# Performance work log

Measured on AMD Instinct MI355X. Metric: run time of the kernel, lower is better.

The kernel has to match this reference:

```python
import jax, jax.numpy as jnp
import numpy as np
from jax.ops import segment_sum, segment_max

N, E, IN_DIM, HID, HEADS, B, ACTIONS = 16384, 262144, 512, 256, 4, 64, 32
NEG_SLOPE = 0.2  # PyG GATConv default leaky-relu slope


def setup_inputs() -> dict:
    key = jax.random.key(0)
    ks = jax.random.split(key, 12)
    x = jax.random.normal(ks[0], (N, IN_DIM), dtype=jnp.float32)
    edge_index = jax.random.randint(ks[1], (2, E), 0, N, dtype=jnp.int64)
    batch = jnp.sort(jax.random.randint(ks[2], (N,), 0, B, dtype=jnp.int64))
    s = 0.05
    return {
        "x": x,
        "edge_index": edge_index,
        "batch": batch,
        # SAGEConv: lin_l (neighbors, with bias) + lin_r (root, no bias)
        "sage_w_l": jax.random.normal(ks[3], (IN_DIM, HID), dtype=jnp.float32) * s,
        "sage_b_l": jnp.zeros((HID,), dtype=jnp.float32),
        "sage_w_r": jax.random.normal(ks[4], (IN_DIM, HID), dtype=jnp.float32) * s,
        # GATConv: shared lin, per-head attention vectors, output bias (concat=False)
        "gat_w": jax.random.normal(ks[5], (HID, HEADS * HID), dtype=jnp.float32) * s,
        "gat_att_src": jax.random.normal(ks[6], (HEADS, HID), dtype=jnp.float32) * s,
        "gat_att_dst": jax.random.normal(ks[7], (HEADS, HID), dtype=jnp.float32) * s,
        "gat_b": jnp.zeros((HID,), dtype=jnp.float32),
        # action head
        "head_w": jax.random.normal(ks[8], (HID, ACTIONS), dtype=jnp.float32) * s,
        "head_b": jnp.zeros((ACTIONS,), dtype=jnp.float32),
    }


def reference(x, edge_index, batch, sage_w_l, sage_b_l, sage_w_r,
              gat_w, gat_att_src, gat_att_dst, gat_b, head_w, head_b):
    src, dst = edge_index[0], edge_index[1]

    # ---- SAGEConv (mean aggregation): lin_l(mean_j x_j) + lin_r(x_i) ----
    agg = segment_sum(x[src], dst, num_segments=N)                 # [N, IN_DIM]
    deg = segment_sum(jnp.ones((E,), x.dtype), dst, num_segments=N)
    mean_nbr = agg / jnp.maximum(deg, 1.0)[:, None]
    h = mean_nbr @ sage_w_l + sage_b_l + x @ sage_w_r              # [N, HID]
    h = jax.nn.relu(h)
    # dropout is identity at inference (training=False)

    # ---- GATConv (adds self-loops, concat=False -> head average) ----
    loop = jnp.arange(N, dtype=src.dtype)
    si = jnp.concatenate([src, loop])                              # [E2]
    di = jnp.concatenate([dst, loop])
    g = (h @ gat_w).reshape(N, HEADS, HID)                         # [N, H, C]
    a_src = jnp.einsum('nhc,hc->nh', g, gat_att_src)               # [N, H]
    a_dst = jnp.einsum('nhc,hc->nh', g, gat_att_dst)
    logits = jax.nn.leaky_relu(a_src[si] + a_dst[di], NEG_SLOPE)   # [E2, H]
    m = segment_max(logits, di, num_segments=N)                    # per-target max
    ex = jnp.exp(logits - m[di])
    denom = segment_sum(ex, di, num_segments=N)
    alpha = ex / denom[di]                                         # [E2, H]
    out = segment_sum(g[si] * alpha[:, :, None], di, num_segments=N)  # [N, H, C]
    out = jax.nn.relu(out.mean(axis=1) + gat_b)                    # [N, HID]

    # ---- global mean pool + action head ----
    pooled = segment_sum(out, batch, num_segments=B)
    cnt = segment_sum(jnp.ones((N,), out.dtype), batch, num_segments=B)
    pooled = pooled / jnp.maximum(cnt, 1.0)[:, None]               # [B, HID]
    return pooled @ head_w + head_b                                # [B, ACTIONS]
```

## Files before the change

kernel.cpp:

```cpp
#include <hip/hip_runtime.h>
#include <math.h>

#define N_NODES 16384
#define N_EDGES 262144
#define IN_DIM  512
#define HID     256
#define HEADS   4
#define NBATCH  64
#define ACTIONS 32
#define NEG_SLOPE 0.2f

typedef __attribute__((ext_vector_type(8))) short short8;
typedef __attribute__((ext_vector_type(4))) float f32x4;

__device__ __forceinline__ float lrelu(float v) { return v > 0.f ? v : NEG_SLOPE * v; }

__device__ __forceinline__ unsigned short bf16_rne(float f) {
    union { float f; unsigned int u; } x; x.f = f;
    unsigned int u = x.u;
    unsigned int r = (u + 0x7FFFu + ((u >> 16) & 1u)) >> 16;
    return (unsigned short)r;
}

__device__ __forceinline__ float bf16_to_f32(unsigned short s) {
    union { unsigned int u; float f; } x; x.u = (unsigned int)s << 16;
    return x.f;
}

__device__ __forceinline__ float4 bf4_to_f4(ushort4 u) {
    return make_float4(bf16_to_f32(u.x), bf16_to_f32(u.y), bf16_to_f32(u.z), bf16_to_f32(u.w));
}

__device__ __forceinline__ void async_copy16(const unsigned short* g, unsigned short* l) {
    __builtin_amdgcn_global_load_lds(
        (const __attribute__((address_space(1))) unsigned int*)g,
        (__attribute__((address_space(3))) unsigned int*)l, 16, 0, 0);
}

#define NB_CONV 8192
#define NB_WLR  1024
#define NB_WSTK 1024
#define NB_WATT 8
#define NB_ZERO 128
#define NB_SETUP (NB_CONV + NB_WLR + NB_WSTK + NB_WATT + NB_ZERO)

__global__ __launch_bounds__(256) void setup_kernel(
        const float* __restrict__ x, unsigned short* __restrict__ xb,
        const float* __restrict__ wl, const float* __restrict__ wr, unsigned short* __restrict__ bt1,
        const float* __restrict__ gat_w, unsigned short* __restrict__ bt2,
        const float* __restrict__ att_src, const float* __restrict__ att_dst, float* __restrict__ watt,
        int* __restrict__ deg, float* __restrict__ pooled) {
    int bid = blockIdx.x, tid = threadIdx.x;
    if (bid < NB_CONV) {
        int i = (bid * 256 + tid) * 4;
        float4 v = *(const float4*)(x + i);
        ushort4 o;
        o.x = bf16_rne(v.x); o.y = bf16_rne(v.y); o.z = bf16_rne(v.z); o.w = bf16_rne(v.w);
        *(ushort4*)(xb + i) = o;
    } else if (bid < NB_CONV + NB_WLR) {
        int idx = (bid - NB_CONV) * 256 + tid;
        int j = idx >> 9;
        int k = idx & 511;
        float v = (j < HID) ? wl[k * HID + j] : wr[k * HID + (j - HID)];
        bt1[idx] = bf16_rne(v);
    } else if (bid < NB_CONV + NB_WLR + NB_WSTK) {
        int idx = (bid - NB_CONV - NB_WLR) * 256 + tid;
        int c = idx >> 10;
        int r = idx & 1023;
        int h = r >> 8;
        int k = r & 255;
        bt2[idx] = bf16_rne(gat_w[(size_t)k * (HEADS * HID) + h * HID + c]);
    } else if (bid < NB_CONV + NB_WLR + NB_WSTK + NB_WATT) {
        int j = bid - NB_CONV - NB_WLR - NB_WSTK;
        int c = tid;
        int hh = j & 3;
        const float* att = (j < 4) ? (att_src + hh * HID) : (att_dst + hh * HID);
        float s = 0.f;
        for (int cc = 0; cc < HID; cc++)
            s += gat_w[(size_t)c * (HEADS * HID) + hh * HID + cc] * att[cc];
        watt[j * HID + c] = s;
    } else {
        int idx = (bid - NB_CONV - NB_WLR - NB_WSTK - NB_WATT) * 256 + tid;
        if (idx < N_NODES) deg[idx] = 0;
        else pooled[idx - N_NODES] = 0.f;
    }
}

__global__ void deg_kernel(const int* __restrict__ ei, int* __restrict__ deg) {
    int e = blockIdx.x * 256 + threadIdx.x;
    if (e < N_EDGES) atomicAdd(&deg[ei[N_EDGES + e]], 1);
}

__global__ __launch_bounds__(256) void scan_kernel(const int* __restrict__ deg,
                                                   int* __restrict__ row_start,
                                                   int* __restrict__ pos) {
    int t = threadIdx.x;
    int lane = t & 63, wv = t >> 6;
    int base = t * 64;
    int4 buf[16];
    int sum = 0;
#pragma unroll
    for (int i = 0; i < 16; i++) {
        buf[i] = ((const int4*)(deg + base))[i];
        sum += buf[i].x + buf[i].y + buf[i].z + buf[i].w;
    }
    int v = sum;
#pragma unroll
    for (int off = 1; off < 64; off <<= 1) {
        int u = __shfl_up(v, off);
        if (lane >= off) v += u;
    }
    __shared__ int wsum[4];
    if (lane == 63) wsum[wv] = v;
    __syncthreads();
    int wbase = 0;
    for (int w0 = 0; w0 < wv; w0++) wbase += wsum[w0];
    int run = wbase + v - sum;
#pragma unroll
    for (int i = 0; i < 16; i++) {
        int4 b = buf[i];
        int4 o;
        o.x = run; run += b.x;
        o.y = run; run += b.y;
        o.z = run; run += b.z;
        o.w = run; run += b.w;
        ((int4*)(row_start + base))[i] = o;
        ((int4*)(pos + base))[i] = o;
    }
    if (t == 255) row_start[N_NODES] = run;
}

__global__ void fill_kernel(const int* __restrict__ ei, int* __restrict__ pos,
                            int* __restrict__ col) {
    int e = blockIdx.x * 256 + threadIdx.x;
    if (e < N_EDGES) {
        int s = ei[e];
        int d = ei[N_EDGES + e];
        int p = atomicAdd(&pos[d], 1);
        col[p] = s;
    }
}

#define BK 32

__global__ __launch_bounds__(256) void gemm1_kernel(const unsigned short* __restrict__ A,
                                                    const unsigned short* __restrict__ Bt,
                                                    unsigned short* __restrict__ Cb,
                                                    int Nn, int K) {
    __shared__ __align__(16) unsigned short As[64 * BK];
    __shared__ __align__(16) unsigned short Bs[128 * BK];

    int tid  = threadIdx.x;
    int wv   = tid >> 6;
    int lane = tid & 63;
    int m0 = blockIdx.y * 64;
    int n0 = blockIdx.x * 128;
    int wm = (wv & 1) * 32;
    int wn = (wv >> 1) * 64;

    int srow = tid >> 2;
    int scol = (tid & 3) * 8;
    const unsigned short* Ag  = A  + (size_t)(m0 + srow) * K + scol;
    const unsigned short* Bg0 = Bt + (size_t)(n0 + srow) * K + scol;
    const unsigned short* Bg1 = Bt + (size_t)(n0 + 64 + srow) * K + scol;
    unsigned short* Al  = As + wv * 512;
    unsigned short* Bl0 = Bs + wv * 512;
    unsigned short* Bl1 = Bs + 2048 + wv * 512;

    int fr = lane & 15;
    int fk = (lane >> 4) * 8;
    f32x4 acc[2][4] = {};

    for (int kt = 0; kt < K; kt += BK) {
        async_copy16(Ag + kt, Al);
        async_copy16(Bg0 + kt, Bl0);
        async_copy16(Bg1 + kt, Bl1);
        __syncthreads();

        short8 af[2], bf[4];
#pragma unroll
        for (int mi = 0; mi < 2; mi++)
            af[mi] = *(const short8*)&As[(wm + mi * 16 + fr) * BK + fk];
#pragma unroll
        for (int ni = 0; ni < 4; ni++)
            bf[ni] = *(const short8*)&Bs[(wn + ni * 16 + fr) * BK + fk];
#pragma unroll
        for (int mi = 0; mi < 2; mi++)
#pragma unroll
            for (int ni = 0; ni < 4; ni++)
                acc[mi][ni] = __builtin_amdgcn_mfma_f32_16x16x32_bf16(af[mi], bf[ni], acc[mi][ni], 0, 0, 0);
        __syncthreads();
    }

    int cr = (lane >> 4) * 4;
    int cc = lane & 15;
#pragma unroll
    for (int mi = 0; mi < 2; mi++) {
#pragma unroll
        for (int ni = 0; ni < 4; ni++) {
            int gc = n0 + wn + ni * 16 + cc;
#pragma unroll
            for (int r = 0; r < 4; r++) {
                int gr = m0 + wm + mi * 16 + cr + r;
                Cb[(size_t)gr * Nn + gc] = bf16_rne(acc[mi][ni][r]);
            }
        }
    }
}

__global__ __launch_bounds__(256) void gemm2_pool_kernel(const unsigned short* __restrict__ A,
                                                         const unsigned short* __restrict__ Bt,
                                                         const int* __restrict__ batch,
                                                         const float* __restrict__ bias,
                                                         float scale,
                                                         float* __restrict__ pooled,
                                                         int Nn, int K) {
    __shared__ __align__(16) unsigned short As[64 * BK];
    __shared__ __align__(16) unsigned short Bs[64 * BK];
    __shared__ int bsh[64];

    int tid  = threadIdx.x;
    int wv   = tid >> 6;
    int lane = tid & 63;
    int m0 = blockIdx.y * 64;
    int n0 = blockIdx.x * 64;
    int wm = (wv & 1) * 32;
    int wn = (wv >> 1) * 32;

    if (tid < 64) bsh[tid] = batch[m0 + tid];

    int srow = tid >> 2;
    int scol = (tid & 3) * 8;
    const unsigned short* Ag = A  + (size_t)(m0 + srow) * K + scol;
    const unsigned short* Bg = Bt + (size_t)(n0 + srow) * K + scol;
    unsigned short* Al = As + wv * 512;
    unsigned short* Bl = Bs + wv * 512;

    int fr = lane & 15;
    int fk = (lane >> 4) * 8;
    f32x4 acc[2][2] = {};

    for (int kt = 0; kt < K; kt += BK) {
        async_copy16(Ag + kt, Al);
        async_copy16(Bg + kt, Bl);
        __syncthreads();

        short8 af[2], bf[2];
#pragma unroll
        for (int mi = 0; mi < 2; mi++)
            af[mi] = *(const short8*)&As[(wm + mi * 16 + fr) * BK + fk];
#pragma unroll
        for (int ni = 0; ni < 2; ni++)
            bf[ni] = *(const short8*)&Bs[(wn + ni * 16 + fr) * BK + fk];
#pragma unroll
        for (int mi = 0; mi < 2; mi++)
#pragma unroll
            for (int ni = 0; ni < 2; ni++)
                acc[mi][ni] = __builtin_amdgcn_mfma_f32_16x16x32_bf16(af[mi], bf[ni], acc[mi][ni], 0, 0, 0);
        __syncthreads();
    }

    int cr = (lane >> 4) * 4;
    int cc = lane & 15;
#pragma unroll
    for (int mi = 0; mi < 2; mi++) {
        int rowb = wm + mi * 16 + cr;
        int b0 = bsh[rowb], b3 = bsh[rowb + 3];
#pragma unroll
        for (int ni = 0; ni < 2; ni++) {
            int gc = n0 + wn + ni * 16 + cc;
            float b = bias[gc];
            float v0 = fmaxf(fmaf(acc[mi][ni][0], scale, b), 0.f);
            float v1 = fmaxf(fmaf(acc[mi][ni][1], scale, b), 0.f);
            float v2 = fmaxf(fmaf(acc[mi][ni][2], scale, b), 0.f);
            float v3 = fmaxf(fmaf(acc[mi][ni][3], scale, b), 0.f);
            if (b0 == b3) {
                atomicAdd(&pooled[b0 * HID + gc], (v0 + v1) + (v2 + v3));
            } else {
                atomicAdd(&pooled[bsh[rowb + 0] * HID + gc], v0);
                atomicAdd(&pooled[bsh[rowb + 1] * HID + gc], v1);
                atomicAdd(&pooled[bsh[rowb + 2] * HID + gc], v2);
                atomicAdd(&pooled[bsh[rowb + 3] * HID + gc], v3);
            }
        }
    }
}

__global__ __launch_bounds__(256) void sage_agg_kernel(const unsigned short* __restrict__ xlr,
                                                       const int* __restrict__ row_start,
                                                       const int* __restrict__ col,
                                                       const float* __restrict__ b_l,
                                                       const float* __restrict__ watt,
                                                       unsigned short* __restrict__ hb,
                                                       float* __restrict__ a_att) {
    __shared__ float watt_s[8 * HID];
    for (int i = threadIdx.x; i < 8 * HID; i += 256) watt_s[i] = watt[i];
    __syncthreads();

    int wave = threadIdx.x >> 6;
    int lane = threadIdx.x & 63;
    int n = blockIdx.x * 4 + wave;
    int start = row_start[n], end = row_start[n + 1];
    int c0 = lane * 4;

    float4 acc = make_float4(0.f, 0.f, 0.f, 0.f);
    int e = start;
    for (; e + 4 <= end; e += 4) {
        int s0 = col[e], s1 = col[e + 1], s2 = col[e + 2], s3 = col[e + 3];
        ushort4 u0 = *(const ushort4*)(xlr + (size_t)s0 * IN_DIM + c0);
        ushort4 u1 = *(const ushort4*)(xlr + (size_t)s1 * IN_DIM + c0);
        ushort4 u2 = *(const ushort4*)(xlr + (size_t)s2 * IN_DIM + c0);
        ushort4 u3 = *(const ushort4*)(xlr + (size_t)s3 * IN_DIM + c0);
        float4 v0 = bf4_to_f4(u0), v1 = bf4_to_f4(u1), v2 = bf4_to_f4(u2), v3 = bf4_to_f4(u3);
        acc.x += (v0.x + v1.x) + (v2.x + v3.x);
        acc.y += (v0.y + v1.y) + (v2.y + v3.y);
        acc.z += (v0.z + v1.z) + (v2.z + v3.z);
        acc.w += (v0.w + v1.w) + (v2.w + v3.w);
    }
    for (; e < end; e++) {
        int s = col[e];
        float4 v = bf4_to_f4(*(const ushort4*)(xlr + (size_t)s * IN_DIM + c0));
        acc.x += v.x; acc.y += v.y; acc.z += v.z; acc.w += v.w;
    }
    float inv = 1.f / (float)max(end - start, 1);
    float4 xr = bf4_to_f4(*(const ushort4*)(xlr + (size_t)n * IN_DIM + HID + c0));
    float4 bl = *(const float4*)(b_l + c0);
    float4 hv;
    hv.x = fmaxf(fmaf(acc.x, inv, bl.x + xr.x), 0.f);
    hv.y = fmaxf(fmaf(acc.y, inv, bl.y + xr.y), 0.f);
    hv.z = fmaxf(fmaf(acc.z, inv, bl.z + xr.z), 0.f);
    hv.w = fmaxf(fmaf(acc.w, inv, bl.w + xr.w), 0.f);
    ushort4 ho;
    ho.x = bf16_rne(hv.x); ho.y = bf16_rne(hv.y); ho.z = bf16_rne(hv.z); ho.w = bf16_rne(hv.w);
    *(ushort4*)(hb + (size_t)n * HID + c0) = ho;

    float p[8];
#pragma unroll
    for (int j = 0; j < 8; j++) {
        float4 wt = *(const float4*)&watt_s[j * HID + c0];
        p[j] = hv.x * wt.x + hv.y * wt.y + hv.z * wt.z + hv.w * wt.w;
    }
#pragma unroll
    for (int off = 32; off; off >>= 1)
#pragma unroll
        for (int j = 0; j < 8; j++) p[j] += __shfl_down(p[j], off);
    if (lane == 0) {
#pragma unroll
        for (int j = 0; j < 8; j++) a_att[n * 8 + j] = p[j];
    }
}

__global__ __launch_bounds__(256) void gat_agg_kernel(const unsigned short* __restrict__ hb,
                                                      const float* __restrict__ a_att,
                                                      const int* __restrict__ row_start,
                                                      const int* __restrict__ col,
                                                      unsigned short* __restrict__ T) {
    __shared__ __align__(16) float w_s[4][64 * 4];
    int wave = threadIdx.x >> 6;
    int lane = threadIdx.x & 63;
    int n = blockIdx.x * 4 + wave;
    int start = row_start[n], end = row_start[n + 1];

    float4 an = *(const float4*)(a_att + n * 8);
    float4 ad = *(const float4*)(a_att + n * 8 + 4);
    float adst[4] = {ad.x, ad.y, ad.z, ad.w};
    float selfl[4] = {lrelu(an.x + ad.x), lrelu(an.y + ad.y), lrelu(an.z + ad.z), lrelu(an.w + ad.w)};
    float m[4], wself[4];
#pragma unroll
    for (int hh = 0; hh < 4; hh++) {
        m[hh] = fmaxf(selfl[hh], 0.f);
        wself[hh] = __expf(selfl[hh] - m[hh]);
    }

    int c0 = lane * 4;
    float4 hn = bf4_to_f4(*(const ushort4*)(hb + (size_t)n * HID + c0));
    float4 acc[4];
#pragma unroll
    for (int hh = 0; hh < 4; hh++)
        acc[hh] = make_float4(wself[hh] * hn.x, wself[hh] * hn.y, wself[hh] * hn.z, wself[hh] * hn.w);

    float dpart[4] = {0.f, 0.f, 0.f, 0.f};

    for (int base = start; base < end; base += 64) {
        int cnt = min(64, end - base);
        if (lane < cnt) {
            int s = col[base + lane];
            float4 as = *(const float4*)(a_att + s * 8);
            float4 wv;
            wv.x = __expf(lrelu(as.x + adst[0]) - m[0]);
            wv.y = __expf(lrelu(as.y + adst[1]) - m[1]);
            wv.z = __expf(lrelu(as.z + adst[2]) - m[2]);
            wv.w = __expf(lrelu(as.w + adst[3]) - m[3]);
            *(float4*)&w_s[wave][lane * 4] = wv;
            dpart[0] += wv.x; dpart[1] += wv.y; dpart[2] += wv.z; dpart[3] += wv.w;
        }
        __builtin_amdgcn_wave_barrier();

        int i = 0;
        for (; i + 2 <= cnt; i += 2) {
            int s0 = col[base + i], s1 = col[base + i + 1];
            float4 w0 = *(const float4*)&w_s[wave][i * 4];
            float4 w1 = *(const float4*)&w_s[wave][(i + 1) * 4];
            ushort4 u0 = *(const ushort4*)(hb + (size_t)s0 * HID + c0);
            ushort4 u1 = *(const ushort4*)(hb + (size_t)s1 * HID + c0);
            float4 h0 = bf4_to_f4(u0), h1 = bf4_to_f4(u1);
            float wr0[4] = {w0.x, w0.y, w0.z, w0.w};
            float wr1[4] = {w1.x, w1.y, w1.z, w1.w};
#pragma unroll
            for (int hh = 0; hh < 4; hh++) {
                acc[hh].x = fmaf(wr0[hh], h0.x, fmaf(wr1[hh], h1.x, acc[hh].x));
                acc[hh].y = fmaf(wr0[hh], h0.y, fmaf(wr1[hh], h1.y, acc[hh].y));
                acc[hh].z = fmaf(wr0[hh], h0.z, fmaf(wr1[hh], h1.z, acc[hh].z));
                acc[hh].w = fmaf(wr0[hh], h0.w, fmaf(wr1[hh], h1.w, acc[hh].w));
            }
        }
        if (i < cnt) {
            int s0 = col[base + i];
            float4 w0 = *(const float4*)&w_s[wave][i * 4];
            float4 h0 = bf4_to_f4(*(const ushort4*)(hb + (size_t)s0 * HID + c0));
            float wr0[4] = {w0.x, w0.y, w0.z, w0.w};
#pragma unroll
            for (int hh = 0; hh < 4; hh++) {
                acc[hh].x = fmaf(wr0[hh], h0.x, acc[hh].x);
                acc[hh].y = fmaf(wr0[hh], h0.y, acc[hh].y);
                acc[hh].z = fmaf(wr0[hh], h0.z, acc[hh].z);
                acc[hh].w = fmaf(wr0[hh], h0.w, acc[hh].w);
            }
        }
        __builtin_amdgcn_wave_barrier();
    }

#pragma unroll
    for (int off = 32; off; off >>= 1)
#pragma unroll
        for (int hh = 0; hh < 4; hh++) dpart[hh] += __shfl_down(dpart[hh], off);
    float invd[4];
#pragma unroll
    for (int hh = 0; hh < 4; hh++)
        invd[hh] = 1.f / (__shfl(dpart[hh], 0) + wself[hh]);

#pragma unroll
    for (int hh = 0; hh < 4; hh++) {
        ushort4 o;
        o.x = bf16_rne(acc[hh].x * invd[hh]); o.y = bf16_rne(acc[hh].y * invd[hh]);
        o.z = bf16_rne(acc[hh].z * invd[hh]); o.w = bf16_rne(acc[hh].w * invd[hh]);
        *(ushort4*)(T + (size_t)n * (HEADS * HID) + hh * HID + c0) = o;
    }
}

__device__ __forceinline__ int lower_bound_i(const int* a, int n, int v) {
    int lo = 0, hi = n;
    while (lo < hi) {
        int mid = (lo + hi) >> 1;
        if (a[mid] < v) lo = mid + 1; else hi = mid;
    }
    return lo;
}

__global__ __launch_bounds__(256) void head_kernel(const float* __restrict__ pooled,
                                                   const int* __restrict__ batch,
                                                   const float* __restrict__ head_w,
                                                   const float* __restrict__ head_b,
                                                   float* __restrict__ out) {
    __shared__ float sm[HID];
    int b = blockIdx.x;
    int c = threadIdx.x;
    int lo = lower_bound_i(batch, N_NODES, b);
    int hi = lower_bound_i(batch, N_NODES, b + 1);
    int cnt = hi - lo;
    sm[c] = pooled[b * HID + c] / (float)max(cnt, 1);
    __syncthreads();
    if (c < ACTIONS) {
        float acc = head_b[c];
        for (int k = 0; k < HID; k++) acc = fmaf(sm[k], head_w[k * ACTIONS + c], acc);
        out[b * ACTIONS + c] = acc;
    }
}

extern "C" void kernel_launch(void* const* d_in, const int* in_sizes, int n_in,
                              void* d_out, int out_size, void* d_ws, size_t ws_size,
                              hipStream_t stream) {
    const float* x        = (const float*)d_in[0];
    const int*   ei       = (const int*)d_in[1];
    const int*   batch    = (const int*)d_in[2];
    const float* sage_w_l = (const float*)d_in[3];
    const float* sage_b_l = (const float*)d_in[4];
    const float* sage_w_r = (const float*)d_in[5];
    const float* gat_w    = (const float*)d_in[6];
    const float* att_src  = (const float*)d_in[7];
    const float* att_dst  = (const float*)d_in[8];
    const float* gat_b    = (const float*)d_in[9];
    const float* head_w   = (const float*)d_in[10];
    const float* head_b   = (const float*)d_in[11];
    float* out = (float*)d_out;

    char* w = (char*)d_ws;
    float* a_att  = (float*)w; w += (size_t)N_NODES * 8 * 4;
    float* watt   = (float*)w; w += (size_t)8 * HID * 4;
    float* pooled = (float*)w; w += (size_t)NBATCH * HID * 4;
    unsigned short* xb  = (unsigned short*)w; w += (size_t)N_NODES * IN_DIM * 2;
    unsigned short* xlr = (unsigned short*)w; w += (size_t)N_NODES * IN_DIM * 2;
    unsigned short* hb  = (unsigned short*)w; w += (size_t)N_NODES * HID * 2;
    unsigned short* T   = (unsigned short*)w; w += (size_t)N_NODES * HEADS * HID * 2;
    unsigned short* bt1 = (unsigned short*)w; w += (size_t)(2 * HID) * IN_DIM * 2;
    unsigned short* bt2 = (unsigned short*)w; w += (size_t)HID * (HEADS * HID) * 2;
    int* deg      = (int*)w;   w += (size_t)N_NODES * 4;
    int* row_start= (int*)w;   w += (size_t)(N_NODES + 64) * 4;
    int* pos      = (int*)w;   w += (size_t)N_NODES * 4;
    int* col      = (int*)w;   w += (size_t)N_EDGES * 4;

    setup_kernel<<<NB_SETUP, 256, 0, stream>>>(x, xb, sage_w_l, sage_w_r, bt1,
                                               gat_w, bt2, att_src, att_dst, watt,
                                               deg, pooled);

    deg_kernel<<<N_EDGES / 256, 256, 0, stream>>>(ei, deg);
    scan_kernel<<<1, 256, 0, stream>>>(deg, row_start, pos);
    fill_kernel<<<N_EDGES / 256, 256, 0, stream>>>(ei, pos, col);

    gemm1_kernel<<<dim3((2 * HID) / 128, N_NODES / 64), 256, 0, stream>>>(
        xb, bt1, xlr, 2 * HID, IN_DIM);

    sage_agg_kernel<<<N_NODES / 4, 256, 0, stream>>>(xlr, row_start, col, sage_b_l, watt, hb, a_att);

    gat_agg_kernel<<<N_NODES / 4, 256, 0, stream>>>(hb, a_att, row_start, col, T);

    gemm2_pool_kernel<<<dim3(HID / 64, N_NODES / 64), 256, 0, stream>>>(
        T, bt2, batch, gat_b, 0.25f, pooled, HID, HEADS * HID);

    head_kernel<<<NBATCH, 256, 0, stream>>>(pooled, batch, head_w, head_b, out);
}
```

Before: 262.4 us.

## Split GEMM2 along K with 128x128 tiles and separate relu-pool pass

Replaces the fused 64x64-tile GEMM2+pool kernel with a split-K GEMM using 128x128 tiles over four K chunks. Partial sums are atomically added into a new fp32 [N,HID] buffer, which is zeroed in the setup kernel. A separate kernel then applies bias, scale and relu and does segmented pooling. The aim is more reuse per tile while keeping enough blocks in flight, at the cost of an extra 16 MB fp32 buffer, heavy global atomics, an extra zeroing pass and an extra launch.

```diff
diff --git a/kernel.cpp b/kernel.cpp
--- a/kernel.cpp
+++ b/kernel.cpp
@@ -42,14 +42,15 @@
 #define NB_WSTK 1024
 #define NB_WATT 8
 #define NB_ZERO 128
-#define NB_SETUP (NB_CONV + NB_WLR + NB_WSTK + NB_WATT + NB_ZERO)
+#define NB_ZOUT 4096
+#define NB_SETUP (NB_CONV + NB_WLR + NB_WSTK + NB_WATT + NB_ZERO + NB_ZOUT)
 
 __global__ __launch_bounds__(256) void setup_kernel(
         const float* __restrict__ x, unsigned short* __restrict__ xb,
         const float* __restrict__ wl, const float* __restrict__ wr, unsigned short* __restrict__ bt1,
         const float* __restrict__ gat_w, unsigned short* __restrict__ bt2,
         const float* __restrict__ att_src, const float* __restrict__ att_dst, float* __restrict__ watt,
-        int* __restrict__ deg, float* __restrict__ pooled) {
+        int* __restrict__ deg, float* __restrict__ pooled, float* __restrict__ outn) {
     int bid = blockIdx.x, tid = threadIdx.x;
     if (bid < NB_CONV) {
         int i = (bid * 256 + tid) * 4;
@@ -79,10 +80,13 @@
         for (int cc = 0; cc < HID; cc++)
             s += gat_w[(size_t)c * (HEADS * HID) + hh * HID + cc] * att[cc];
         watt[j * HID + c] = s;
-    } else {
+    } else if (bid < NB_CONV + NB_WLR + NB_WSTK + NB_WATT + NB_ZERO) {
         int idx = (bid - NB_CONV - NB_WLR - NB_WSTK - NB_WATT) * 256 + tid;
         if (idx < N_NODES) deg[idx] = 0;
         else pooled[idx - N_NODES] = 0.f;
+    } else {
+        int i = ((bid - NB_CONV - NB_WLR - NB_WSTK - NB_WATT - NB_ZERO) * 256 + tid) * 4;
+        *(float4*)(outn + i) = make_float4(0.f, 0.f, 0.f, 0.f);
     }
 }
 
@@ -208,54 +212,57 @@
     }
 }
 
-__global__ __launch_bounds__(256) void gemm2_pool_kernel(const unsigned short* __restrict__ A,
-                                                         const unsigned short* __restrict__ Bt,
-                                                         const int* __restrict__ batch,
-                                                         const float* __restrict__ bias,
-                                                         float scale,
-                                                         float* __restrict__ pooled,
-                                                         int Nn, int K) {
-    __shared__ __align__(16) unsigned short As[64 * BK];
-    __shared__ __align__(16) unsigned short Bs[64 * BK];
-    __shared__ int bsh[64];
+#define KCHUNK 256
+
+__global__ __launch_bounds__(256) void gemm2_splitk_kernel(const unsigned short* __restrict__ A,
+                                                           const unsigned short* __restrict__ Bt,
+                                                           float* __restrict__ outn,
+                                                           int Nn, int K) {
+    __shared__ __align__(16) unsigned short As[128 * BK];
+    __shared__ __align__(16) unsigned short Bs[128 * BK];
 
     int tid  = threadIdx.x;
     int wv   = tid >> 6;
     int lane = tid & 63;
-    int m0 = blockIdx.y * 64;
-    int n0 = blockIdx.x * 64;
-    int wm = (wv & 1) * 32;
-    int wn = (wv >> 1) * 32;
-
-    if (tid < 64) bsh[tid] = batch[m0 + tid];
+    int m0 = blockIdx.y * 128;
+    int n0 = blockIdx.x * 128;
+    int k0 = blockIdx.z * KCHUNK;
+    int wm = (wv & 1) * 64;
+    int wn = (wv >> 1) * 64;
 
     int srow = tid >> 2;
     int scol = (tid & 3) * 8;
-    const unsigned short* Ag = A  + (size_t)(m0 + srow) * K + scol;
-    const unsigned short* Bg = Bt + (size_t)(n0 + srow) * K + scol;
-    unsigned short* Al = As + wv * 512;
-    unsigned short* Bl = Bs + wv * 512;
+    const unsigned short* Ag0 = A  + (size_t)(m0 + srow) * K + k0 + scol;
+    const unsigned short* Ag1 = A  + (size_t)(m0 + 64 + srow) * K + k0 + scol;
+    const unsigned short* Bg0 = Bt + (size_t)(n0 + srow) * K + k0 + scol;
+    const unsigned short* Bg1 = Bt + (size_t)(n0 + 64 + srow) * K + k0 + scol;
+    unsigned short* Al0 = As + wv * 512;
+    unsigned short* Al1 = As + 2048 + wv * 512;
+    unsigned short* Bl0 = Bs + wv * 512;
+    unsigned short* Bl1 = Bs + 2048 + wv * 512;
 
     int fr = lane & 15;
     int fk = (lane >> 4) * 8;
-    f32x4 acc[2][2] = {};
-
-    for (int kt = 0; kt < K; kt += BK) {
-        async_copy16(Ag + kt, Al);
-        async_copy16(Bg + kt, Bl);
+    f32x4 acc[4][4] = {};
+
+    for (int kt = 0; kt < KCHUNK; kt += BK) {
+        async_copy16(Ag0 + kt, Al0);
+        async_copy16(Ag1 + kt, Al1);
+        async_copy16(Bg0 + kt, Bl0);
+        async_copy16(Bg1 + kt, Bl1);
         __syncthreads();
 
-        short8 af[2], bf[2];
-#pragma unroll
-        for (int mi = 0; mi < 2; mi++)
+        short8 af[4], bf[4];
+#pragma unroll
+        for (int mi = 0; mi < 4; mi++)
             af[mi] = *(const short8*)&As[(wm + mi * 16 + fr) * BK + fk];
 #pragma unroll
-        for (int ni = 0; ni < 2; ni++)
+        for (int ni = 0; ni < 4; ni++)
             bf[ni] = *(const short8*)&Bs[(wn + ni * 16 + fr) * BK + fk];
 #pragma unroll
-        for (int mi = 0; mi < 2; mi++)
-#pragma unroll
-            for (int ni = 0; ni < 2; ni++)
+        for (int mi = 0; mi < 4; mi++)
+#pragma unroll
+            for (int ni = 0; ni < 4; ni++)
                 acc[mi][ni] = __builtin_amdgcn_mfma_f32_16x16x32_bf16(af[mi], bf[ni], acc[mi][ni], 0, 0, 0);
         __syncthreads();
     }
@@ -263,27 +270,40 @@
     int cr = (lane >> 4) * 4;
     int cc = lane & 15;
 #pragma unroll
-    for (int mi = 0; mi < 2; mi++) {
-        int rowb = wm + mi * 16 + cr;
-        int b0 = bsh[rowb], b3 = bsh[rowb + 3];
-#pragma unroll
-        for (int ni = 0; ni < 2; ni++) {
+    for (int mi = 0; mi < 4; mi++) {
+#pragma unroll
+        for (int ni = 0; ni < 4; ni++) {
             int gc = n0 + wn + ni * 16 + cc;
-            float b = bias[gc];
-            float v0 = fmaxf(fmaf(acc[mi][ni][0], scale, b), 0.f);
-            float v1 = fmaxf(fmaf(acc[mi][ni][1], scale, b), 0.f);
-            float v2 = fmaxf(fmaf(acc[mi][ni][2], scale, b), 0.f);
-            float v3 = fmaxf(fmaf(acc[mi][ni][3], scale, b), 0.f);
-            if (b0 == b3) {
-                atomicAdd(&pooled[b0 * HID + gc], (v0 + v1) + (v2 + v3));
-            } else {
-                atomicAdd(&pooled[bsh[rowb + 0] * HID + gc], v0);
-                atomicAdd(&pooled[bsh[rowb + 1] * HID + gc], v1);
-                atomicAdd(&pooled[bsh[rowb + 2] * HID + gc], v2);
-                atomicAdd(&pooled[bsh[rowb + 3] * HID + gc], v3);
+#pragma unroll
+            for (int r = 0; r < 4; r++) {
+                int gr = m0 + wm + mi * 16 + cr + r;
+                atomicAdd(&outn[(size_t)gr * Nn + gc], acc[mi][ni][r]);
             }
         }
     }
+}
+
+__global__ __launch_bounds__(256) void relu_pool_kernel(const float* __restrict__ outn,
+                                                        const int* __restrict__ batch,
+                                                        const float* __restrict__ bias,
+                                                        float scale,
+                                                        float* __restrict__ pooled) {
+    int c = threadIdx.x;
+    int n0 = blockIdx.x * 64;
+    float b = bias[c];
+    int cur = batch[n0];
+    float acc = 0.f;
+    for (int i = 0; i < 64; i++) {
+        int n = n0 + i;
+        int bb = batch[n];
+        if (bb != cur) {
+            atomicAdd(&pooled[cur * HID + c], acc);
+            acc = 0.f;
+            cur = bb;
+        }
+        acc += fmaxf(fmaf(outn[(size_t)n * HID + c], scale, b), 0.f);
+    }
+    atomicAdd(&pooled[cur * HID + c], acc);
 }
 
 __global__ __launch_bounds__(256) void sage_agg_kernel(const unsigned short* __restrict__ xlr,
@@ -498,6 +518,7 @@
     float* a_att  = (float*)w; w += (size_t)N_NODES * 8 * 4;
     float* watt   = (float*)w; w += (size_t)8 * HID * 4;
     float* pooled = (float*)w; w += (size_t)NBATCH * HID * 4;
+    float* outn   = (float*)w; w += (size_t)N_NODES * HID * 4;
     unsigned short* xb  = (unsigned short*)w; w += (size_t)N_NODES * IN_DIM * 2;
     unsigned short* xlr = (unsigned short*)w; w += (size_t)N_NODES * IN_DIM * 2;
     unsigned short* hb  = (unsigned short*)w; w += (size_t)N_NODES * HID * 2;
@@ -511,7 +532,7 @@
 
     setup_kernel<<<NB_SETUP, 256, 0, stream>>>(x, xb, sage_w_l, sage_w_r, bt1,
                                                gat_w, bt2, att_src, att_dst, watt,
-                                               deg, pooled);
+                                               deg, pooled, outn);
 
     deg_kernel<<<N_EDGES / 256, 256, 0, stream>>>(ei, deg);
     scan_kernel<<<1, 256, 0, stream>>>(deg, row_start, pos);
@@ -524,8 +545,10 @@
 
     gat_agg_kernel<<<N_NODES / 4, 256, 0, stream>>>(hb, a_att, row_start, col, T);
 
-    gemm2_pool_kernel<<<dim3(HID / 64, N_NODES / 64), 256, 0, stream>>>(
-        T, bt2, batch, gat_b, 0.25f, pooled, HID, HEADS * HID);
+    gemm2_splitk_kernel<<<dim3(HID / 128, N_NODES / 128, 4), 256, 0, stream>>>(
+        T, bt2, outn, HID, HEADS * HID);
+
+    relu_pool_kernel<<<N_NODES / 64, 256, 0, stream>>>(outn, batch, gat_b, 0.25f, pooled);
 
     head_kernel<<<NBATCH, 256, 0, stream>>>(pooled, batch, head_w, head_b, out);
 }
```

Result: slower. 306.5 us (+16.8%).
